# Optimization experiments

Hardware: AMD Instinct MI355X
Metric: run time of the kernel (lower is better)

Reference implementation:

```python
import jax, jax.numpy as jnp
import numpy as np

N = 100000   # nodes
E = 1600000  # edges (avg degree 16)
D = 128      # input = hidden = out dim
L = 4        # num_layers
EPS = 1e-5   # LayerNorm eps


def setup_inputs() -> dict:
    key = jax.random.key(0)
    k0, k1, k2, k3, k4 = jax.random.split(key, 5)
    in_feat = jax.random.normal(k0, (N, D), dtype=jnp.float32)
    edge_index = jax.random.randint(k1, (2, E), 0, N, dtype=jnp.int32)
    s = 1.0 / np.sqrt(D)
    # GraphConv params per layer: lin_rel (weight+bias), lin_root (weight, no bias)
    W_rel = jax.random.uniform(k2, (L, D, D), jnp.float32, -s, s)
    b_rel = jax.random.uniform(k3, (L, D), jnp.float32, -s, s)
    W_root = jax.random.uniform(k4, (L, D, D), jnp.float32, -s, s)
    # single shared LayerNorm module in the torch code
    ln_gamma = jnp.ones((D,), jnp.float32)
    ln_beta = jnp.zeros((D,), jnp.float32)
    return {"in_feat": in_feat, "edge_index": edge_index, "W_rel": W_rel,
            "b_rel": b_rel, "W_root": W_root, "ln_gamma": ln_gamma, "ln_beta": ln_beta}


def _layer_norm(h, gamma, beta):
    mu = jnp.mean(h, axis=-1, keepdims=True)
    var = jnp.mean(jnp.square(h - mu), axis=-1, keepdims=True)
    return (h - mu) * jax.lax.rsqrt(var + EPS) * gamma + beta


def _graph_conv(h, W_r, b_r, W_rt, src, dst):
    # PyG GraphConv: out_i = lin_rel(sum_{j->i} x_j) + lin_root(x_i)
    agg = jax.ops.segment_sum(h[src], dst, num_segments=N)  # [N, D]
    return agg @ W_r + b_r + h @ W_rt


def reference(in_feat, edge_index, W_rel, b_rel, W_root, ln_gamma, ln_beta):
    src, dst = edge_index[0], edge_index[1]
    # input layer: conv -> ReLU -> LayerNorm -> dropout(p=0)
    h = _graph_conv(in_feat, W_rel[0], b_rel[0], W_root[0], src, dst)
    h = _layer_norm(jax.nn.relu(h), ln_gamma, ln_beta)
    # middle layers with residual
    for l in range(1, L - 1):
        nh = _graph_conv(h, W_rel[l], b_rel[l], W_root[l], src, dst)
        h = _layer_norm(jax.nn.relu(nh + h), ln_gamma, ln_beta)
    # output layer: conv only
    return _graph_conv(h, W_rel[L - 1], b_rel[L - 1], W_root[L - 1], src, dst)
```

## Files before the change

kernel.cpp:

```cpp
#include <hip/hip_runtime.h>
#include <cstddef>

#define N_NODES 100000
#define N_PAD   100032
#define N_EDGES 1600000
#define DIM 128
#define LN_EPS 1e-5f
#define ZROW   N_NODES
#define COL_CAP 3200000

#define B_SHIFT 9
#define B_SIZE  512
#define N_BKT   196
#define EPB     4096
#define NBLK    ((N_EDGES + EPB - 1) / EPB)

typedef short bf16x8 __attribute__((ext_vector_type(8)));
typedef float f32x4 __attribute__((ext_vector_type(4)));
typedef float f32x2 __attribute__((ext_vector_type(2)));

__device__ __forceinline__ float asf(uint u) {
    union { uint i; float f; } c; c.i = u; return c.f;
}
__device__ __forceinline__ float bf2f(uint u) { return asf(u << 16); }
__device__ __forceinline__ ushort f2bf(float x) {
    union { float f; uint i; } c; c.f = x;
    uint r = c.i + 0x7fffu + ((c.i >> 16) & 1u);
    return (ushort)(r >> 16);
}

__device__ __forceinline__ void accp(f32x2* acc, uint p) {
    f32x2 v;
    v.x = asf(p << 16);
    v.y = asf(p & 0xffff0000u);
    *acc += v;
}
__device__ __forceinline__ void accq(f32x2* a, uint4 p) {
    accp(&a[0], p.x); accp(&a[1], p.y); accp(&a[2], p.z); accp(&a[3], p.w);
}


__global__ __launch_bounds__(256) void bhist_kernel(const int* __restrict__ dst,
                                                    int* __restrict__ bcount) {
    __shared__ int lh[N_BKT];
    const int tid = threadIdx.x;
    if (tid < N_BKT) lh[tid] = 0;
    __syncthreads();
    const int base = blockIdx.x * EPB;
    #pragma unroll
    for (int k = 0; k < 16; ++k) {
        int t = base + tid + k * 256;
        if (t < N_EDGES) atomicAdd(&lh[dst[t] >> B_SHIFT], 1);
    }
    __syncthreads();
    if (tid < N_BKT && lh[tid]) atomicAdd(&bcount[tid], lh[tid]);
}

__global__ __launch_bounds__(256) void bscan_kernel(const int* __restrict__ bcount,
                                                    int* __restrict__ bstart,
                                                    int* __restrict__ gcur) {
    __shared__ int s[256];
    const int tid = threadIdx.x;
    int v = (tid < N_BKT) ? bcount[tid] : 0;
    s[tid] = v;
    __syncthreads();
    for (int off = 1; off < 256; off <<= 1) {
        int t = (tid >= off) ? s[tid - off] : 0;
        __syncthreads();
        s[tid] += t;
        __syncthreads();
    }
    if (tid < N_BKT) { int e = s[tid] - v; bstart[tid] = e; gcur[tid] = e; }
    if (tid == 0) bstart[N_BKT] = N_EDGES;
}

__global__ __launch_bounds__(256) void bscatter_kernel(const int* __restrict__ src,
                                                       const int* __restrict__ dst,
                                                       int* __restrict__ gcur,
                                                       int2* __restrict__ pairs) {
    __shared__ int lcnt[N_BKT];
    __shared__ int lbase[N_BKT];
    const int tid = threadIdx.x;
    if (tid < N_BKT) lcnt[tid] = 0;
    __syncthreads();
    const int base = blockIdx.x * EPB;
    int ls[16], ld[16];
    #pragma unroll
    for (int k = 0; k < 16; ++k) {
        int t = base + tid + k * 256;
        if (t < N_EDGES) {
            ls[k] = src[t]; ld[k] = dst[t];
            atomicAdd(&lcnt[ld[k] >> B_SHIFT], 1);
        } else ld[k] = -1;
    }
    __syncthreads();
    if (tid < N_BKT) lbase[tid] = lcnt[tid] ? atomicAdd(&gcur[tid], lcnt[tid]) : 0;
    __syncthreads();
    if (tid < N_BKT) lcnt[tid] = 0;
    __syncthreads();
    #pragma unroll
    for (int k = 0; k < 16; ++k) {
        if (ld[k] >= 0) {
            int b = ld[k] >> B_SHIFT;
            int r = atomicAdd(&lcnt[b], 1);
            pairs[lbase[b] + r] = make_int2(ls[k], ld[k]);
        }
    }
}

__global__ __launch_bounds__(256) void ndeg_kernel(const int2* __restrict__ pairs,
                                                   const int* __restrict__ bstart,
                                                   int* __restrict__ row_ptr,
                                                   int* __restrict__ bpad) {
    __shared__ int ldeg[B_SIZE];
    __shared__ int ws4[4];
    const int b = blockIdx.x;
    const int node0 = b << B_SHIFT;
    const int tid = threadIdx.x;
    ldeg[tid] = 0; ldeg[tid + 256] = 0;
    __syncthreads();
    const int beg = bstart[b], end = bstart[b + 1];
    for (int t = beg + tid; t < end; t += 256)
        atomicAdd(&ldeg[pairs[t].y - node0], 1);
    __syncthreads();
    const int d0 = (ldeg[2 * tid] + 15) & ~15;
    const int d1 = (ldeg[2 * tid + 1] + 15) & ~15;
    const int sum2 = d0 + d1;
    const int lane = tid & 63, wv = tid >> 6;
    int incl = sum2;
    #pragma unroll
    for (int off = 1; off < 64; off <<= 1) {
        int t = __shfl_up(incl, off);
        if (lane >= off) incl += t;
    }
    if (lane == 63) ws4[wv] = incl;
    __syncthreads();
    int woff = 0;
    if (wv > 0) woff += ws4[0];
    if (wv > 1) woff += ws4[1];
    if (wv > 2) woff += ws4[2];
    const int e0 = woff + incl - sum2;
    const int n0 = node0 + 2 * tid;
    if (n0 < N_NODES)     row_ptr[n0]     = e0;
    if (n0 + 1 < N_NODES) row_ptr[n0 + 1] = e0 + d0;
    if (tid == 255) bpad[b] = woff + incl;
}

__global__ __launch_bounds__(256) void pscan_kernel(const int* __restrict__ bpad,
                                                    int* __restrict__ bpadstart) {
    __shared__ int s[256];
    const int tid = threadIdx.x;
    int v = (tid < N_BKT) ? bpad[tid] : 0;
    s[tid] = v;
    __syncthreads();
    for (int off = 1; off < 256; off <<= 1) {
        int t = (tid >= off) ? s[tid - off] : 0;
        __syncthreads();
        s[tid] += t;
        __syncthreads();
    }
    if (tid < N_BKT) bpadstart[tid] = s[tid] - v;
    if (tid == N_BKT - 1) bpadstart[N_BKT] = s[tid];
}

__global__ void addbase_kernel(int* __restrict__ row_ptr, const int* __restrict__ bpadstart) {
    int n = blockIdx.x * 256 + threadIdx.x;
    if (n < N_NODES) row_ptr[n] += bpadstart[n >> B_SHIFT];
    else if (n <= N_PAD) row_ptr[n] = bpadstart[N_BKT];
}

__global__ __launch_bounds__(256) void bfill_kernel(const int2* __restrict__ pairs,
                                                    const int* __restrict__ bstart,
                                                    const int* __restrict__ row_ptr,
                                                    int* __restrict__ col) {
    __shared__ int lcur[B_SIZE];
    const int b = blockIdx.x;
    const int node0 = b << B_SHIFT;
    const int tid = threadIdx.x;
    #pragma unroll
    for (int k = 0; k < 2; ++k) {
        int n = node0 + tid + k * 256;
        lcur[tid + k * 256] = (n < N_NODES) ? row_ptr[n] : 0;
    }
    __syncthreads();
    const int beg = bstart[b], end = bstart[b + 1];
    for (int t = beg + tid; t < end; t += 256) {
        int2 p = pairs[t];
        int r = atomicAdd(&lcur[p.y - node0], 1);
        col[r] = p.x;
    }
    __syncthreads();
    #pragma unroll
    for (int k = 0; k < 2; ++k) {
        int n = tid + k * 256;
        int node = node0 + n;
        if (node < N_NODES) {
            int e = lcur[n];
            int pe = row_ptr[node + 1];
            for (int p = e; p < pe; ++p) col[p] = ZROW;
        }
    }
}


__global__ void cvt_kernel(const float* __restrict__ in, ushort* __restrict__ out) {
    int i = (blockIdx.x * blockDim.x + threadIdx.x) * 4;
    float4 v = *(const float4*)&in[i];
    uint2 r;
    r.x = (uint)f2bf(v.x) | ((uint)f2bf(v.y) << 16);
    r.y = (uint)f2bf(v.z) | ((uint)f2bf(v.w) << 16);
    *(uint2*)&out[i] = r;
}


__global__ void prepack_kernel(const float* __restrict__ Wrel, const float* __restrict__ Wroot,
                               ushort* __restrict__ Wp) {
    int t = blockIdx.x * blockDim.x + threadIdx.x;
    int layer = t >> 12;
    int m = (t >> 11) & 1;
    int frag = (t >> 6) & 31;
    int lane = t & 63;
    int ks = frag >> 3, n = frag & 7;
    int c = n * 16 + (lane & 15);
    int k0 = ks * 32 + (lane >> 4) * 8;
    ushort tmp[8];
    #pragma unroll
    for (int j = 0; j < 8; ++j) {
        int k = k0 + j;
        float w;
        if (m == 0) {
            w = Wrel[layer * 16384 + k * 128 + c];
        } else {
            w = Wroot[layer * 16384 + k * 128 + c];
            if ((layer == 1 || layer == 2) && k == c) w += 1.0f;
        }
        tmp[j] = f2bf(w);
    }
    *(uint4*)&Wp[(size_t)t * 8] = *(const uint4*)tmp;
}


template <int MODE>
__global__ __launch_bounds__(256, 6) void fused_kernel(const ushort* __restrict__ hb,
                                                       const int* __restrict__ row_ptr,
                                                       const int* __restrict__ col,
                                                       const ushort* __restrict__ Wp,
                                                       const float* __restrict__ brel,
                                                       const float* __restrict__ gamma,
                                                       const float* __restrict__ beta,
                                                       ushort* __restrict__ outb,
                                                       float* __restrict__ outf) {
    __shared__ char sA[64 * 256];
    const int tid = threadIdx.x;
    const int row0 = blockIdx.x * 64;
    const int lane = tid & 63;
    const int wv = tid >> 6;
    const int rsel = lane >> 4;
    const int c16 = lane & 15;

    const uint4* h4 = (const uint4*)hb;
    #pragma unroll 1
    for (int t = 0; t < 8; ++t) {
        const int rA = wv * 16 + 2 * t;
        const int rB = rA + 1;
        const int p0 = row_ptr[row0 + rA];
        const int p1 = row_ptr[row0 + rA + 1];
        const int p2 = row_ptr[row0 + rA + 2];
        const int itA = (p1 - p0) >> 4;
        const int itB = (p2 - p1) >> 4;
        int jA = p0 + rsel;
        int jB = p1 + rsel;
        const int iters = max(itA, itB);

        f32x2 a[4], b[4];
        #pragma unroll
        for (int u = 0; u < 4; ++u) { a[u] = (f32x2){0.f, 0.f}; b[u] = (f32x2){0.f, 0.f}; }

        for (int it = 0; it < iters; ++it) {
            int sA0 = ZROW, sA1 = ZROW, sA2 = ZROW, sA3 = ZROW;
            int sB0 = ZROW, sB1 = ZROW, sB2 = ZROW, sB3 = ZROW;
            if (it < itA) {
                sA0 = col[jA]; sA1 = col[jA + 4]; sA2 = col[jA + 8]; sA3 = col[jA + 12];
                jA += 16;
            }
            if (it < itB) {
                sB0 = col[jB]; sB1 = col[jB + 4]; sB2 = col[jB + 8]; sB3 = col[jB + 12];
                jB += 16;
            }
            uint4 pA0 = h4[(size_t)sA0 * 16 + c16];
            uint4 pA1 = h4[(size_t)sA1 * 16 + c16];
            uint4 pA2 = h4[(size_t)sA2 * 16 + c16];
            uint4 pA3 = h4[(size_t)sA3 * 16 + c16];
            uint4 pB0 = h4[(size_t)sB0 * 16 + c16];
            uint4 pB1 = h4[(size_t)sB1 * 16 + c16];
            uint4 pB2 = h4[(size_t)sB2 * 16 + c16];
            uint4 pB3 = h4[(size_t)sB3 * 16 + c16];
            accq(a, pA0); accq(a, pA1); accq(a, pA2); accq(a, pA3);
            accq(b, pB0); accq(b, pB1); accq(b, pB2); accq(b, pB3);
        }

        #pragma unroll
        for (int u = 0; u < 4; ++u) {
            float ax = a[u].x, ay = a[u].y, bx = b[u].x, by = b[u].y;
            ax += __shfl_xor(ax, 16); ay += __shfl_xor(ay, 16);
            bx += __shfl_xor(bx, 16); by += __shfl_xor(by, 16);
            ax += __shfl_xor(ax, 32); ay += __shfl_xor(ay, 32);
            bx += __shfl_xor(bx, 32); by += __shfl_xor(by, 32);
            a[u].x = ax; a[u].y = ay; b[u].x = bx; b[u].y = by;
        }
        if (rsel == 0) {
            uint4 o;
            o.x = (uint)f2bf(a[0].x) | ((uint)f2bf(a[0].y) << 16);
            o.y = (uint)f2bf(a[1].x) | ((uint)f2bf(a[1].y) << 16);
            o.z = (uint)f2bf(a[2].x) | ((uint)f2bf(a[2].y) << 16);
            o.w = (uint)f2bf(a[3].x) | ((uint)f2bf(a[3].y) << 16);
            *(uint4*)&sA[rA * 256 + ((c16 * 16) ^ ((rA & 7) << 4))] = o;
        } else if (rsel == 1) {
            uint4 o;
            o.x = (uint)f2bf(b[0].x) | ((uint)f2bf(b[0].y) << 16);
            o.y = (uint)f2bf(b[1].x) | ((uint)f2bf(b[1].y) << 16);
            o.z = (uint)f2bf(b[2].x) | ((uint)f2bf(b[2].y) << 16);
            o.w = (uint)f2bf(b[3].x) | ((uint)f2bf(b[3].y) << 16);
            *(uint4*)&sA[rB * 256 + ((c16 * 16) ^ ((rB & 7) << 4))] = o;
        }
    }
    __syncthreads();

    const int kg = lane >> 4;
    const int cl = lane & 15;
    const int ra = wv * 16 + cl;
    const size_t growa = (size_t)row0 + ra;
    const int abase = ra * 256 + kg * 16;
    const int aswz = (ra & 7) << 4;

    f32x4 acc[8];
    #pragma unroll
    for (int n = 0; n < 8; ++n) acc[n] = (f32x4){0.f, 0.f, 0.f, 0.f};

    const uint4* bR = (const uint4*)Wp + lane;
    const uint4* bT = (const uint4*)(Wp + 16384) + lane;
    #pragma unroll
    for (int ks = 0; ks < 4; ++ks) {
        bf16x8 a = *(const bf16x8*)&sA[(abase + ks * 64) ^ aswz];
        #pragma unroll
        for (int n = 0; n < 8; ++n) {
            bf16x8 b = *(const bf16x8*)&bR[(ks * 8 + n) * 64];
            acc[n] = __builtin_amdgcn_mfma_f32_16x16x32_bf16(a, b, acc[n], 0, 0, 0);
        }
    }
    #pragma unroll
    for (int ks = 0; ks < 4; ++ks) {
        bf16x8 a = *(const bf16x8*)&hb[growa * 128 + ks * 32 + kg * 8];
        #pragma unroll
        for (int n = 0; n < 8; ++n) {
            bf16x8 b = *(const bf16x8*)&bT[(ks * 8 + n) * 64];
            acc[n] = __builtin_amdgcn_mfma_f32_16x16x32_bf16(a, b, acc[n], 0, 0, 0);
        }
    }

    float bias[8], gg[8], bb[8];
    #pragma unroll
    for (int n = 0; n < 8; ++n) {
        int cn = n * 16 + cl;
        bias[n] = brel[cn];
        if (MODE != 2) { gg[n] = gamma[cn]; bb[n] = beta[cn]; }
    }

    #pragma unroll
    for (int reg = 0; reg < 4; ++reg) {
        const int r = wv * 16 + kg * 4 + reg;
        const size_t grow = (size_t)row0 + r;
        const bool live = grow < N_NODES;
        float v[8];
        float s = 0.f, q = 0.f;
        #pragma unroll
        for (int n = 0; n < 8; ++n) {
            float x = acc[n][reg] + bias[n];
            if (MODE != 2) x = fmaxf(x, 0.f);
            v[n] = x; s += x; q += x * x;
        }
        if (MODE != 2) {
            #pragma unroll
            for (int m = 8; m >= 1; m >>= 1) { s += __shfl_xor(s, m); q += __shfl_xor(q, m); }
            float mu = s * (1.f / DIM);
            float var = q * (1.f / DIM) - mu * mu;
            float rinv = rsqrtf(var + LN_EPS);
            if (live) {
                #pragma unroll
                for (int n = 0; n < 8; ++n) {
                    float y = (v[n] - mu) * rinv * gg[n] + bb[n];
                    outb[grow * DIM + n * 16 + cl] = f2bf(y);
                }
            }
        } else {
            if (live) {
                #pragma unroll
                for (int n = 0; n < 8; ++n) outf[grow * DIM + n * 16 + cl] = v[n];
            }
        }
    }
}


static inline size_t align256(size_t x) { return (x + 255) & ~(size_t)255; }

extern "C" void kernel_launch(void* const* d_in, const int* in_sizes, int n_in,
                              void* d_out, int out_size, void* d_ws, size_t ws_size,
                              hipStream_t stream) {
    const float* in_feat = (const float*)d_in[0];
    const int*   ei      = (const int*)d_in[1];
    const float* Wrel    = (const float*)d_in[2];
    const float* brel    = (const float*)d_in[3];
    const float* Wroot   = (const float*)d_in[4];
    const float* gamma   = (const float*)d_in[5];
    const float* beta    = (const float*)d_in[6];
    float* out = (float*)d_out;

    char* ws = (char*)d_ws;
    size_t off = 0;
    int* col = (int*)(ws + off);        off = align256(off + (size_t)COL_CAP * 4);
    int2* pairs = (int2*)(ws + off);    off = align256(off + (size_t)N_EDGES * 8);
    int* row_ptr = (int*)(ws + off);    off = align256(off + (size_t)(N_PAD + 2) * 4);
    int* bcount = (int*)(ws + off);     off = align256(off + (size_t)N_BKT * 4);
    int* bstart = (int*)(ws + off);     off = align256(off + (size_t)(N_BKT + 1) * 4);
    int* gcur = (int*)(ws + off);       off = align256(off + (size_t)N_BKT * 4);
    int* bpad = (int*)(ws + off);       off = align256(off + (size_t)N_BKT * 4);
    int* bpadstart = (int*)(ws + off);  off = align256(off + (size_t)(N_BKT + 1) * 4);
    ushort* x0 = (ushort*)(ws + off);   off = align256(off + (size_t)N_PAD * DIM * 2);
    ushort* hA = (ushort*)(ws + off);   off = align256(off + (size_t)N_PAD * DIM * 2);
    ushort* hB = (ushort*)(ws + off);   off = align256(off + (size_t)N_PAD * DIM * 2);
    ushort* Wp = (ushort*)(ws + off);   off = align256(off + (size_t)4 * 2 * 128 * 128 * 2);
    (void)ws_size; (void)in_sizes; (void)n_in; (void)out_size;

    const int* src = ei;
    const int* dst = ei + N_EDGES;

    hipMemsetAsync(bcount, 0, (size_t)N_BKT * 4, stream);
    bhist_kernel<<<NBLK, 256, 0, stream>>>(dst, bcount);
    bscan_kernel<<<1, 256, 0, stream>>>(bcount, bstart, gcur);
    bscatter_kernel<<<NBLK, 256, 0, stream>>>(src, dst, gcur, pairs);
    ndeg_kernel<<<N_BKT, 256, 0, stream>>>(pairs, bstart, row_ptr, bpad);
    pscan_kernel<<<1, 256, 0, stream>>>(bpad, bpadstart);
    addbase_kernel<<<(N_PAD + 1 + 255) / 256, 256, 0, stream>>>(row_ptr, bpadstart);
    bfill_kernel<<<N_BKT, 256, 0, stream>>>(pairs, bstart, row_ptr, col);

    const size_t padoff = (size_t)N_NODES * DIM * 2;
    const size_t padlen = (size_t)(N_PAD - N_NODES) * DIM * 2;
    hipMemsetAsync((char*)x0 + padoff, 0, padlen, stream);
    hipMemsetAsync((char*)hA + padoff, 0, padlen, stream);
    hipMemsetAsync((char*)hB + padoff, 0, padlen, stream);

    cvt_kernel<<<(N_NODES * DIM) / (4 * 256), 256, 0, stream>>>(in_feat, x0);
    prepack_kernel<<<64, 256, 0, stream>>>(Wrel, Wroot, Wp);

    const int grid = N_PAD / 64;

    fused_kernel<0><<<grid, 256, 0, stream>>>(x0, row_ptr, col, Wp, brel, gamma, beta, hA, nullptr);
    fused_kernel<0><<<grid, 256, 0, stream>>>(hA, row_ptr, col, Wp + 32768, brel + DIM, gamma, beta, hB, nullptr);
    fused_kernel<0><<<grid, 256, 0, stream>>>(hB, row_ptr, col, Wp + 2 * 32768, brel + 2 * DIM, gamma, beta, hA, nullptr);
    fused_kernel<2><<<grid, 256, 0, stream>>>(hA, row_ptr, col, Wp + 3 * 32768, brel + 3 * DIM, gamma, beta, nullptr, out);
}
```

Before: 449.2 us.

## Use 512-thread blocks splitting output columns across wave pairs with LDS LayerNorm reduction

Doubles the fused GraphConv block to 8 waves. Each wave now gathers 8 rows instead of 16, and the MFMA output is split so each wave computes half the 128 columns for 16 rows. Because a row's LayerNorm statistics now span two waves, partial sums are exchanged through a small LDS buffer with an extra barrier. The normalized bf16 output is staged in LDS and written back as coalesced 16-byte stores. The aim is more parallelism for hiding gather latency and fewer accumulator registers per thread, at the cost of extra block-wide synchronization.

```diff
diff --git a/kernel.cpp b/kernel.cpp
--- a/kernel.cpp
+++ b/kernel.cpp
@@ -241,7 +241,7 @@
 
 
 template <int MODE>
-__global__ __launch_bounds__(256, 6) void fused_kernel(const ushort* __restrict__ hb,
+__global__ __launch_bounds__(512, 8) void fused_kernel(const ushort* __restrict__ hb,
                                                        const int* __restrict__ row_ptr,
                                                        const int* __restrict__ col,
                                                        const ushort* __restrict__ Wp,
@@ -251,6 +251,7 @@
                                                        ushort* __restrict__ outb,
                                                        float* __restrict__ outf) {
     __shared__ char sA[64 * 256];
+    __shared__ float2 lnbuf[64][2];
     const int tid = threadIdx.x;
     const int row0 = blockIdx.x * 64;
     const int lane = tid & 63;
@@ -260,8 +261,8 @@
 
     const uint4* h4 = (const uint4*)hb;
     #pragma unroll 1
-    for (int t = 0; t < 8; ++t) {
-        const int rA = wv * 16 + 2 * t;
+    for (int t = 0; t < 4; ++t) {
+        const int rA = wv * 8 + 2 * t;
         const int rB = rA + 1;
         const int p0 = row_ptr[row0 + rA];
         const int p1 = row_ptr[row0 + rA + 1];
@@ -328,14 +329,16 @@
 
     const int kg = lane >> 4;
     const int cl = lane & 15;
-    const int ra = wv * 16 + cl;
+    const int rh = wv & 3;
+    const int ch = wv >> 2;
+    const int ra = rh * 16 + cl;
     const size_t growa = (size_t)row0 + ra;
     const int abase = ra * 256 + kg * 16;
     const int aswz = (ra & 7) << 4;
 
-    f32x4 acc[8];
-    #pragma unroll
-    for (int n = 0; n < 8; ++n) acc[n] = (f32x4){0.f, 0.f, 0.f, 0.f};
+    f32x4 acc[4];
+    #pragma unroll
+    for (int n = 0; n < 4; ++n) acc[n] = (f32x4){0.f, 0.f, 0.f, 0.f};
 
     const uint4* bR = (const uint4*)Wp + lane;
     const uint4* bT = (const uint4*)(Wp + 16384) + lane;
@@ -343,8 +346,8 @@
     for (int ks = 0; ks < 4; ++ks) {
         bf16x8 a = *(const bf16x8*)&sA[(abase + ks * 64) ^ aswz];
         #pragma unroll
-        for (int n = 0; n < 8; ++n) {
-            bf16x8 b = *(const bf16x8*)&bR[(ks * 8 + n) * 64];
+        for (int n = 0; n < 4; ++n) {
+            bf16x8 b = *(const bf16x8*)&bR[(ks * 8 + ch * 4 + n) * 64];
             acc[n] = __builtin_amdgcn_mfma_f32_16x16x32_bf16(a, b, acc[n], 0, 0, 0);
         }
     }
@@ -352,50 +355,75 @@
     for (int ks = 0; ks < 4; ++ks) {
         bf16x8 a = *(const bf16x8*)&hb[growa * 128 + ks * 32 + kg * 8];
         #pragma unroll
-        for (int n = 0; n < 8; ++n) {
-            bf16x8 b = *(const bf16x8*)&bT[(ks * 8 + n) * 64];
+        for (int n = 0; n < 4; ++n) {
+            bf16x8 b = *(const bf16x8*)&bT[(ks * 8 + ch * 4 + n) * 64];
             acc[n] = __builtin_amdgcn_mfma_f32_16x16x32_bf16(a, b, acc[n], 0, 0, 0);
         }
     }
 
-    float bias[8], gg[8], bb[8];
-    #pragma unroll
-    for (int n = 0; n < 8; ++n) {
-        int cn = n * 16 + cl;
+    float bias[4], gg[4], bb[4];
+    #pragma unroll
+    for (int n = 0; n < 4; ++n) {
+        int cn = ch * 64 + n * 16 + cl;
         bias[n] = brel[cn];
         if (MODE != 2) { gg[n] = gamma[cn]; bb[n] = beta[cn]; }
     }
 
-    #pragma unroll
-    for (int reg = 0; reg < 4; ++reg) {
-        const int r = wv * 16 + kg * 4 + reg;
-        const size_t grow = (size_t)row0 + r;
-        const bool live = grow < N_NODES;
-        float v[8];
-        float s = 0.f, q = 0.f;
-        #pragma unroll
-        for (int n = 0; n < 8; ++n) {
-            float x = acc[n][reg] + bias[n];
-            if (MODE != 2) x = fmaxf(x, 0.f);
-            v[n] = x; s += x; q += x * x;
-        }
-        if (MODE != 2) {
+    if (MODE != 2) {
+        float vv[4][4];
+        float ss[4], qq[4];
+        #pragma unroll
+        for (int reg = 0; reg < 4; ++reg) {
+            float s = 0.f, q = 0.f;
+            #pragma unroll
+            for (int n = 0; n < 4; ++n) {
+                float x = acc[n][reg] + bias[n];
+                x = fmaxf(x, 0.f);
+                vv[reg][n] = x; s += x; q += x * x;
+            }
             #pragma unroll
             for (int m = 8; m >= 1; m >>= 1) { s += __shfl_xor(s, m); q += __shfl_xor(q, m); }
+            ss[reg] = s; qq[reg] = q;
+        }
+        if (cl == 0) {
+            #pragma unroll
+            for (int reg = 0; reg < 4; ++reg)
+                lnbuf[rh * 16 + kg * 4 + reg][ch] = make_float2(ss[reg], qq[reg]);
+        }
+        __syncthreads();
+        ushort* so = (ushort*)sA;
+        #pragma unroll
+        for (int reg = 0; reg < 4; ++reg) {
+            const int r = rh * 16 + kg * 4 + reg;
+            float2 e0 = lnbuf[r][0], e1 = lnbuf[r][1];
+            float s = e0.x + e1.x;
+            float q = e0.y + e1.y;
             float mu = s * (1.f / DIM);
             float var = q * (1.f / DIM) - mu * mu;
             float rinv = rsqrtf(var + LN_EPS);
-            if (live) {
+            #pragma unroll
+            for (int n = 0; n < 4; ++n) {
+                float y = (vv[reg][n] - mu) * rinv * gg[n] + bb[n];
+                so[r * 128 + ch * 64 + n * 16 + cl] = f2bf(y);
+            }
+        }
+        __syncthreads();
+        #pragma unroll
+        for (int t2 = tid; t2 < 1024; t2 += 512) {
+            int r = t2 >> 4, cc = t2 & 15;
+            size_t grow = (size_t)row0 + r;
+            if (grow < N_NODES)
+                *(uint4*)&outb[grow * DIM + cc * 8] = *(const uint4*)&sA[r * 256 + cc * 16];
+        }
+    } else {
+        #pragma unroll
+        for (int reg = 0; reg < 4; ++reg) {
+            const int r = rh * 16 + kg * 4 + reg;
+            const size_t grow = (size_t)row0 + r;
+            if (grow < N_NODES) {
                 #pragma unroll
-                for (int n = 0; n < 8; ++n) {
-                    float y = (v[n] - mu) * rinv * gg[n] + bb[n];
-                    outb[grow * DIM + n * 16 + cl] = f2bf(y);
-                }
-            }
-        } else {
-            if (live) {
-                #pragma unroll
-                for (int n = 0; n < 8; ++n) outf[grow * DIM + n * 16 + cl] = v[n];
+                for (int n = 0; n < 4; ++n)
+                    outf[grow * DIM + ch * 64 + n * 16 + cl] = acc[n][reg] + bias[n];
             }
         }
     }
@@ -455,8 +483,8 @@
 
     const int grid = N_PAD / 64;
 
-    fused_kernel<0><<<grid, 256, 0, stream>>>(x0, row_ptr, col, Wp, brel, gamma, beta, hA, nullptr);
-    fused_kernel<0><<<grid, 256, 0, stream>>>(hA, row_ptr, col, Wp + 32768, brel + DIM, gamma, beta, hB, nullptr);
-    fused_kernel<0><<<grid, 256, 0, stream>>>(hB, row_ptr, col, Wp + 2 * 32768, brel + 2 * DIM, gamma, beta, hA, nullptr);
-    fused_kernel<2><<<grid, 256, 0, stream>>>(hA, row_ptr, col, Wp + 3 * 32768, brel + 3 * DIM, gamma, beta, nullptr, out);
-}
+    fused_kernel<0><<<grid, 512, 0, stream>>>(x0, row_ptr, col, Wp, brel, gamma, beta, hA, nullptr);
+    fused_kernel<0><<<grid, 512, 0, stream>>>(hA, row_ptr, col, Wp + 32768, brel + DIM, gamma, beta, hB, nullptr);
+    fused_kernel<0><<<grid, 512, 0, stream>>>(hB, row_ptr, col, Wp + 2 * 32768, brel + 2 * DIM, gamma, beta, hA, nullptr);
+    fused_kernel<2><<<grid, 512, 0, stream>>>(hA, row_ptr, col, Wp + 3 * 32768, brel + 3 * DIM, gamma, beta, nullptr, out);
+}
```

New measurement: 468.8 us. 1.04x slower.
